# Optimization experiments

Measured on AMD Instinct MI355X. Metric: run time of the kernel, lower is better.

## Reference

```python
import jax, jax.numpy as jnp
import numpy as np

D_MODEL = 2048
NUM_HEADS = 16
D_Q = 1536
D_KV = 512
BS, SL = 2, 2048


def _lin(x, w, b):
    # torch nn.Linear: y = x @ w.T + b, w: [out, in]
    return jnp.einsum('...i,oi->...o', x, w) + b


def _freqs(seq_len, dim, theta=10000.0):
    # Faithful to source incl. precedence quirk: tn = 1 / ((theta ** arange) / dim).
    # float32 overflow -> inf -> tn = 0 for large exponents (identity rotation).
    exps = jnp.arange(0, dim, 2, dtype=jnp.float32)
    tn = 1.0 / ((theta ** exps) / dim)
    m = jnp.arange(seq_len, dtype=jnp.float32)
    ang = jnp.outer(m, tn)  # [sl, dim/2]
    return jnp.cos(ang), jnp.sin(ang)


def _rope(x, cos, sin):
    # x: [bs, sl, dim]; complex pairs are (x[..., 2i], x[..., 2i+1])
    xe = x[..., 0::2]
    xo = x[..., 1::2]
    re = xe * cos - xo * sin
    im = xe * sin + xo * cos
    return jnp.stack([re, im], axis=-1).reshape(x.shape)


def _init_linear(key, out_f, in_f):
    k1, k2 = jax.random.split(key)
    bound = 1.0 / np.sqrt(in_f)
    w = jax.random.uniform(k1, (out_f, in_f), jnp.float32, -bound, bound)
    b = jax.random.uniform(k2, (out_f,), jnp.float32, -bound, bound)
    return w, b


def setup_inputs() -> dict:
    key = jax.random.key(0)
    ks = jax.random.split(key, 9)
    x = jax.random.normal(ks[0], (BS, SL, D_MODEL), jnp.float32)
    w_down_q, b_down_q = _init_linear(ks[1], D_Q, D_MODEL)
    w_up_q, b_up_q = _init_linear(ks[2], D_MODEL, D_Q)
    w_down_kv, b_down_kv = _init_linear(ks[3], D_KV, D_MODEL)
    w_up_k, b_up_k = _init_linear(ks[4], D_MODEL, D_KV)
    w_up_v, b_up_v = _init_linear(ks[5], D_MODEL, D_KV)
    wq_r, bq_r = _init_linear(ks[6], D_MODEL, D_Q)
    wk_r, bk_r = _init_linear(ks[7], D_MODEL, D_KV)
    wo, bo = _init_linear(ks[8], D_MODEL, D_MODEL)
    return dict(x=x,
                w_down_q=w_down_q, b_down_q=b_down_q,
                w_up_q=w_up_q, b_up_q=b_up_q,
                w_down_kv=w_down_kv, b_down_kv=b_down_kv,
                w_up_k=w_up_k, b_up_k=b_up_k,
                w_up_v=w_up_v, b_up_v=b_up_v,
                wq_r=wq_r, bq_r=bq_r,
                wk_r=wk_r, bk_r=bk_r,
                wo=wo, bo=bo)


def reference(x, w_down_q, b_down_q, w_up_q, b_up_q, w_down_kv, b_down_kv,
              w_up_k, b_up_k, w_up_v, b_up_v, wq_r, bq_r, wk_r, bk_r, wo, bo):
    bs, sl, dim = x.shape
    nh, hd = NUM_HEADS, dim // NUM_HEADS
    cos, sin = _freqs(sl, dim)

    # Query path: down-proj -> up-proj content + decoupled RoPE branch
    ct_q = _lin(x, w_down_q, b_down_q)                       # [bs, sl, d_q]
    q_ct = _lin(ct_q, w_up_q, b_up_q)                        # [bs, sl, d_model]
    rope_q = _rope(_lin(ct_q, wq_r, bq_r), cos, sin)         # [bs, sl, d_model]
    q = (q_ct + rope_q).reshape(bs, sl, nh, hd)

    # KV path: shared latent -> separate K/V up-proj + RoPE branch on K
    ct_kv = _lin(x, w_down_kv, b_down_kv)                    # [bs, sl, d_kv]
    k_ct = _lin(ct_kv, w_up_k, b_up_k)
    rope_k = _rope(_lin(ct_kv, wk_r, bk_r), cos, sin)
    k = (k_ct + rope_k).reshape(bs, sl, nh, hd)
    v = _lin(ct_kv, w_up_v, b_up_v).reshape(bs, sl, nh, hd)

    # Attention: explicit matmul + softmax + matmul (no causal mask in source)
    scores = jnp.einsum('bqhd,bkhd->bhqk', q, k) / np.sqrt(hd)
    probs = jax.nn.softmax(scores, axis=-1)
    a = jnp.einsum('bhqk,bkhd->bqhd', probs, v).reshape(bs, sl, nh * hd)
    return _lin(a, wo, bo)
```

## Files before the change

### kernel.cpp

```cpp
#include <hip/hip_runtime.h>

typedef float f32x4 __attribute__((ext_vector_type(4)));
typedef unsigned short us8 __attribute__((ext_vector_type(8)));

#define DEVINL __device__ __forceinline__

DEVINL unsigned short f2bf(float f) {
  unsigned u = __builtin_bit_cast(unsigned, f);
  u += 0x7fffu + ((u >> 16) & 1u);
  return (unsigned short)(u >> 16);
}
DEVINL float bf2f(unsigned short b) { return __builtin_bit_cast(float, ((unsigned)b) << 16); }
DEVINL us8 ld8(const unsigned short* p) { return *reinterpret_cast<const us8*>(p); }
DEVINL void mfma_bf16(f32x4& acc, us8 a, us8 b) {
  asm("v_mfma_f32_16x16x32_bf16 %0, %1, %2, %0" : "+v"(acc) : "v"(a), "v"(b));
}
DEVINL unsigned cvtpk_bf16(float lo, float hi) {
  unsigned r;
  asm("v_cvt_pk_bf16_f32 %0, %1, %2" : "=v"(r) : "v"(lo), "v"(hi));
  return r;
}
DEVINL void gld16(const void* g, void* l) {
  __builtin_amdgcn_global_load_lds((const __attribute__((address_space(1))) void*)g,
                                   (__attribute__((address_space(3))) void*)l, 16, 0, 0);
}

__global__ void k_cvt(const float* __restrict__ in, unsigned short* __restrict__ out, int n4) {
  int i = blockIdx.x * 256 + threadIdx.x;
  if (i >= n4) return;
  float4 v = reinterpret_cast<const float4*>(in)[i];
  unsigned lo = (unsigned)f2bf(v.x) | ((unsigned)f2bf(v.y) << 16);
  unsigned hi = (unsigned)f2bf(v.z) | ((unsigned)f2bf(v.w) << 16);
  reinterpret_cast<uint2*>(out)[i] = make_uint2(lo, hi);
}

__global__ void k_freqs(float* __restrict__ cosT, float* __restrict__ sinT) {
  int idx = blockIdx.x * 256 + threadIdx.x;
  if (idx >= 2048 * 1024) return;
  int s = idx >> 10, i = idx & 1023;
  float e = (float)(2 * i);
  float pw = powf(10000.0f, e);
  float tn = 1.0f / (pw / 2048.0f);
  float ang = (float)s * tn;
  cosT[idx] = cosf(ang);
  sinT[idx] = sinf(ang);
}

template <bool OUTF32>
__global__ __launch_bounds__(256) void k_gemm_bt(const unsigned short* __restrict__ A,
                                                 const unsigned short* __restrict__ B,
                                                 const float* __restrict__ bias,
                                                 void* __restrict__ Cout, int M, int N, int K,
                                                 int lda) {
  __shared__ unsigned short As[128 * 32];
  __shared__ unsigned short Bs[128 * 32];
  const int nwg = gridDim.x;
  const int q8 = nwg >> 3;
  const int orig = blockIdx.x;
  const int wgid = (orig & 7) * q8 + (orig >> 3);
  const int nbn = N >> 7;
  const int bn = wgid % nbn, bm = wgid / nbn;
  const int tid = threadIdx.x, lane = tid & 63, w = tid >> 6;
  const int g = lane >> 4, l16 = lane & 15;
  const int wm = w >> 1, wn = w & 1;
  f32x4 acc[4][4] = {};
  const unsigned short* Arow = A + (size_t)bm * 128 * lda;
  const unsigned short* Brow = B + (size_t)bn * 128 * K;
  for (int kt = 0; kt < K; kt += 32) {
    __syncthreads();
#pragma unroll
    for (int j = 0; j < 2; ++j) {
      int c = (j * 4 + w) * 64 + lane;
      int row = c >> 2, c4 = c & 3;
      gld16(&Arow[(size_t)row * lda + kt + c4 * 8], &As[(j * 4 + w) * 64 * 8]);
      gld16(&Brow[(size_t)row * K + kt + c4 * 8], &Bs[(j * 4 + w) * 64 * 8]);
    }
    __syncthreads();
    us8 af[4], bfg[4];
#pragma unroll
    for (int mm = 0; mm < 4; ++mm) af[mm] = ld8(&As[(wm * 64 + mm * 16 + l16) * 32 + g * 8]);
#pragma unroll
    for (int nn = 0; nn < 4; ++nn) bfg[nn] = ld8(&Bs[(wn * 64 + nn * 16 + l16) * 32 + g * 8]);
#pragma unroll
    for (int mm = 0; mm < 4; ++mm)
#pragma unroll
      for (int nn = 0; nn < 4; ++nn) mfma_bf16(acc[mm][nn], af[mm], bfg[nn]);
  }
#pragma unroll
  for (int nn = 0; nn < 4; ++nn) {
    int col = bn * 128 + wn * 64 + nn * 16 + l16;
    float bv = bias[col];
#pragma unroll
    for (int mm = 0; mm < 4; ++mm) {
      int row0 = bm * 128 + wm * 64 + mm * 16 + g * 4;
#pragma unroll
      for (int r = 0; r < 4; ++r) {
        float vv = acc[mm][nn][r] + bv;
        if (OUTF32)
          reinterpret_cast<float*>(Cout)[(size_t)(row0 + r) * N + col] = vv;
        else
          reinterpret_cast<unsigned short*>(Cout)[(size_t)(row0 + r) * N + col] = f2bf(vv);
      }
    }
  }
}

__global__ void k_rope_combine(const unsigned short* __restrict__ src, int ldin,
                               const float* __restrict__ cosT, const float* __restrict__ sinT,
                               unsigned short* __restrict__ outp) {
  int pidx = blockIdx.x * 256 + threadIdx.x;
  if (pidx >= 4096 * 1024) return;
  int row = pidx >> 10, i = pidx & 1023;
  int s = row & 2047;
  float c = cosT[s * 1024 + i], sn = sinT[s * 1024 + i];
  const unsigned short* rp = src + (size_t)row * ldin;
  float xe = bf2f(rp[2048 + 2 * i]), xo = bf2f(rp[2048 + 2 * i + 1]);
  float re = xe * c - xo * sn;
  float im = xe * sn + xo * c;
  float q0 = bf2f(rp[2 * i]) + re;
  float q1 = bf2f(rp[2 * i + 1]) + im;
  unsigned pack = (unsigned)f2bf(q0) | ((unsigned)f2bf(q1) << 16);
  *reinterpret_cast<unsigned*>(&outp[(size_t)row * 2048 + 2 * i]) = pack;
}

__global__ __launch_bounds__(256) void k_transpose_v(const unsigned short* __restrict__ v, int ld,
                                                     unsigned short* __restrict__ vt) {
  __shared__ unsigned short t[32][33];
  int tx = threadIdx.x & 31, ty = threadIdx.x >> 5;
  int r0 = blockIdx.y * 32, c0 = blockIdx.x * 32;
#pragma unroll
  for (int jj = 0; jj < 4; ++jj)
    t[ty * 4 + jj][tx] = v[(size_t)(r0 + ty * 4 + jj) * ld + c0 + tx];
  __syncthreads();
  int b = r0 >> 11;
#pragma unroll
  for (int jj = 0; jj < 4; ++jj) {
    int colc = c0 + ty * 4 + jj;
    size_t orow = (size_t)(b * 16 + (colc >> 7)) * 128 + (colc & 127);
    vt[orow * 2048 + (r0 & 2047) + tx] = t[tx][ty * 4 + jj];
  }
}

__global__ __launch_bounds__(256, 2) void k_attn(const unsigned short* __restrict__ Q,
                                                 const unsigned short* __restrict__ Kg,
                                                 const unsigned short* __restrict__ VT,
                                                 unsigned short* __restrict__ Aout) {
  __shared__ unsigned short Ks[64 * 128];
  __shared__ unsigned short VTs[128 * 64];
  __shared__ unsigned short Ps[4][2][16 * 64];
  const int tid = threadIdx.x, lane = tid & 63, w = tid >> 6;
  const int g = lane >> 4, l16 = lane & 15;
  const int qt = blockIdx.x, h = blockIdx.y, b = blockIdx.z;
  const float SC2 = 0.08838834764831845f * 1.4426950408889634f;
  us8 qf[2][4];
#pragma unroll
  for (int qg = 0; qg < 2; ++qg) {
    const size_t qrow = (size_t)b * 2048 + qt * 128 + w * 32 + qg * 16 + l16;
#pragma unroll
    for (int kc = 0; kc < 4; ++kc)
      qf[qg][kc] = ld8(&Q[qrow * 2048 + h * 128 + kc * 32 + g * 8]);
  }
  f32x4 O[2][8] = {};
  float mq[2] = {-1e30f, -1e30f}, lq[2] = {0.f, 0.f};
  const unsigned short* Kbase = Kg + (size_t)b * 2048 * 2048 + h * 128;
  const unsigned short* VTb = VT + (size_t)(b * 16 + h) * 128 * 2048;
  for (int kt = 0; kt < 2048; kt += 64) {
    __syncthreads();
#pragma unroll
    for (int j = 0; j < 4; ++j) {
      int ch = (j * 4 + w) * 64 + lane;
      int key = ch >> 4, cp = ch & 15;
      gld16(&Kbase[(size_t)(kt + key) * 2048 + (size_t)((cp ^ (key & 7)) * 8)],
            &Ks[(j * 4 + w) * 64 * 8]);
      int d = ch >> 3, c2 = ch & 7;
      gld16(&VTb[(size_t)d * 2048 + kt + (size_t)((c2 ^ (d & 7)) * 8)],
            &VTs[(j * 4 + w) * 64 * 8]);
    }
    __syncthreads();
    f32x4 st[2][4] = {};
    __builtin_amdgcn_s_setprio(1);
#pragma unroll
    for (int t = 0; t < 4; ++t) {
      int key = t * 16 + l16;
      int swz = (key & 7) << 3;
#pragma unroll
      for (int kc = 0; kc < 4; ++kc) {
        us8 kf = ld8(&Ks[key * 128 + ((kc * 32 + g * 8) ^ swz)]);
        mfma_bf16(st[0][t], kf, qf[0][kc]);
        mfma_bf16(st[1][t], kf, qf[1][kc]);
      }
    }
    __builtin_amdgcn_s_setprio(0);
    const int qswz = (l16 & 7) << 3;
#pragma unroll
    for (int qg = 0; qg < 2; ++qg) {
      float sv[16];
      float smax = -1e30f;
#pragma unroll
      for (int t = 0; t < 4; ++t)
#pragma unroll
        for (int r = 0; r < 4; ++r) {
          sv[t * 4 + r] = st[qg][t][r] * SC2;
          smax = fmaxf(smax, sv[t * 4 + r]);
        }
      smax = fmaxf(smax, __shfl_xor(smax, 16));
      smax = fmaxf(smax, __shfl_xor(smax, 32));
      float mn = fmaxf(mq[qg], smax);
      float fac = exp2f(mq[qg] - mn);
      float ps = 0.f;
#pragma unroll
      for (int i = 0; i < 16; ++i) {
        sv[i] = exp2f(sv[i] - mn);
        ps += sv[i];
      }
      ps += __shfl_xor(ps, 16);
      ps += __shfl_xor(ps, 32);
      lq[qg] = lq[qg] * fac + ps;
      mq[qg] = mn;
#pragma unroll
      for (int r = 0; r < 4; ++r) {
        float fr = __shfl(fac, g * 4 + r);
#pragma unroll
        for (int n0 = 0; n0 < 8; ++n0) O[qg][n0][r] *= fr;
      }
      unsigned* P32 = reinterpret_cast<unsigned*>(&Ps[w][qg][0]);
#pragma unroll
      for (int t = 0; t < 4; ++t)
#pragma unroll
        for (int pp = 0; pp < 2; ++pp) {
          int key = t * 16 + g * 4 + pp * 2;
          unsigned pk = cvtpk_bf16(sv[t * 4 + pp * 2], sv[t * 4 + pp * 2 + 1]);
          int elem = l16 * 64 + (key ^ qswz);
          P32[elem >> 1] = pk;
        }
    }
    us8 pf[2][2];
#pragma unroll
    for (int qg = 0; qg < 2; ++qg)
#pragma unroll
      for (int kc = 0; kc < 2; ++kc)
        pf[qg][kc] = ld8(&Ps[w][qg][l16 * 64 + ((kc * 32 + g * 8) ^ qswz)]);
    __builtin_amdgcn_s_setprio(1);
#pragma unroll
    for (int n0 = 0; n0 < 8; ++n0) {
      int d = n0 * 16 + l16;
      int dsw = (d & 7) << 3;
#pragma unroll
      for (int kc = 0; kc < 2; ++kc) {
        us8 vf = ld8(&VTs[d * 64 + ((kc * 32 + g * 8) ^ dsw)]);
        mfma_bf16(O[0][n0], pf[0][kc], vf);
        mfma_bf16(O[1][n0], pf[1][kc], vf);
      }
    }
    __builtin_amdgcn_s_setprio(0);
  }
#pragma unroll
  for (int qg = 0; qg < 2; ++qg) {
    float inv = 1.0f / lq[qg];
#pragma unroll
    for (int r = 0; r < 4; ++r) {
      float ir = __shfl(inv, g * 4 + r);
      size_t row = (size_t)b * 2048 + qt * 128 + w * 32 + qg * 16 + g * 4 + r;
#pragma unroll
      for (int n0 = 0; n0 < 8; ++n0)
        Aout[row * 2048 + h * 128 + n0 * 16 + l16] = f2bf(O[qg][n0][r] * ir);
    }
  }
}

extern "C" void kernel_launch(void* const* d_in, const int* in_sizes, int n_in, void* d_out,
                              int out_size, void* d_ws, size_t ws_size, hipStream_t stream) {
  (void)in_sizes; (void)n_in; (void)out_size; (void)ws_size;
  constexpr int Mr = 4096;
  using US = unsigned short;
  const float* x        = (const float*)d_in[0];
  const float* w_down_q = (const float*)d_in[1];
  const float* b_down_q = (const float*)d_in[2];
  const float* w_up_q   = (const float*)d_in[3];
  const float* b_up_q   = (const float*)d_in[4];
  const float* w_down_kv= (const float*)d_in[5];
  const float* b_down_kv= (const float*)d_in[6];
  const float* w_up_k   = (const float*)d_in[7];
  const float* b_up_k   = (const float*)d_in[8];
  const float* w_up_v   = (const float*)d_in[9];
  const float* b_up_v   = (const float*)d_in[10];
  const float* wq_r     = (const float*)d_in[11];
  const float* bq_r     = (const float*)d_in[12];
  const float* wk_r     = (const float*)d_in[13];
  const float* bk_r     = (const float*)d_in[14];
  const float* wo       = (const float*)d_in[15];
  const float* bo       = (const float*)d_in[16];

  char* p = (char*)d_ws;
  auto alloc = [&](size_t bytes) { char* r = p; p += (bytes + 255) & ~(size_t)255; return r; };
  float* cosT = (float*)alloc((size_t)2048 * 1024 * 4);
  float* sinT = (float*)alloc((size_t)2048 * 1024 * 4);
  US* xb        = (US*)alloc((size_t)Mr * 2048 * 2);
  US* wcat_down = (US*)alloc((size_t)2048 * 2048 * 2);
  US* wcat_qup  = (US*)alloc((size_t)4096 * 1536 * 2);
  US* wcat_kvup = (US*)alloc((size_t)6144 * 512 * 2);
  US* wob       = (US*)alloc((size_t)2048 * 2048 * 2);
  US* ct        = (US*)alloc((size_t)Mr * 2048 * 2);
  US* big       = (US*)alloc((size_t)Mr * 6144 * 2);
  US* vtb       = (US*)alloc((size_t)Mr * 2048 * 2);
  float* bcat_down = (float*)alloc(2048 * 4);
  float* bcat_qup  = (float*)alloc(4096 * 4);
  float* bcat_kvup = (float*)alloc(6144 * 4);
  US* qb   = xb;
  US* kb   = wcat_down;
  US* t12  = big;
  US* kv3  = big;
  US* aout = ct;

  auto cvt = [&](const float* s, US* dptr, size_t n) {
    int n4 = (int)(n / 4);
    k_cvt<<<dim3((n4 + 255) / 256), dim3(256), 0, stream>>>(s, dptr, n4);
  };
  cvt(x, xb, (size_t)Mr * 2048);
  cvt(w_down_q, wcat_down, (size_t)1536 * 2048);
  cvt(w_down_kv, wcat_down + (size_t)1536 * 2048, (size_t)512 * 2048);
  cvt(w_up_q, wcat_qup, (size_t)2048 * 1536);
  cvt(wq_r, wcat_qup + (size_t)2048 * 1536, (size_t)2048 * 1536);
  cvt(w_up_k, wcat_kvup, (size_t)2048 * 512);
  cvt(wk_r, wcat_kvup + (size_t)2048 * 512, (size_t)2048 * 512);
  cvt(w_up_v, wcat_kvup + (size_t)4096 * 512, (size_t)2048 * 512);
  cvt(wo, wob, (size_t)2048 * 2048);
  hipMemcpyAsync(bcat_down, b_down_q, 1536 * 4, hipMemcpyDeviceToDevice, stream);
  hipMemcpyAsync(bcat_down + 1536, b_down_kv, 512 * 4, hipMemcpyDeviceToDevice, stream);
  hipMemcpyAsync(bcat_qup, b_up_q, 2048 * 4, hipMemcpyDeviceToDevice, stream);
  hipMemcpyAsync(bcat_qup + 2048, bq_r, 2048 * 4, hipMemcpyDeviceToDevice, stream);
  hipMemcpyAsync(bcat_kvup, b_up_k, 2048 * 4, hipMemcpyDeviceToDevice, stream);
  hipMemcpyAsync(bcat_kvup + 2048, bk_r, 2048 * 4, hipMemcpyDeviceToDevice, stream);
  hipMemcpyAsync(bcat_kvup + 4096, b_up_v, 2048 * 4, hipMemcpyDeviceToDevice, stream);
  k_freqs<<<dim3((2048 * 1024 + 255) / 256), dim3(256), 0, stream>>>(cosT, sinT);

  auto gemm_bf = [&](const US* A, const US* B, const float* bias, US* C, int M, int N, int K,
                     int lda) {
    k_gemm_bt<false><<<dim3((N / 128) * (M / 128)), dim3(256), 0, stream>>>(A, B, bias, (void*)C,
                                                                            M, N, K, lda);
  };
  gemm_bf(xb, wcat_down, bcat_down, ct, Mr, 2048, 2048, 2048);
  gemm_bf(ct, wcat_qup, bcat_qup, t12, Mr, 4096, 1536, 2048);
  k_rope_combine<<<dim3((4096 * 1024 + 255) / 256), dim3(256), 0, stream>>>(t12, 4096, cosT, sinT,
                                                                            qb);
  gemm_bf(ct + 1536, wcat_kvup, bcat_kvup, kv3, Mr, 6144, 512, 2048);
  k_rope_combine<<<dim3((4096 * 1024 + 255) / 256), dim3(256), 0, stream>>>(kv3, 6144, cosT, sinT,
                                                                            kb);
  k_transpose_v<<<dim3(64, 128), dim3(256), 0, stream>>>(kv3 + 4096, 6144, vtb);
  k_attn<<<dim3(16, 16, 2), dim3(256), 0, stream>>>(qb, kb, vtb, aout);
  k_gemm_bt<true><<<dim3((2048 / 128) * (Mr / 128)), dim3(256), 0, stream>>>(aout, wob, bo, d_out,
                                                                             Mr, 2048, 2048, 2048);
}
```

Before: 412.0 us.

## Double-buffer attention K/V, lazy softmax rescale, fold scale into Q, narrower GEMM tiles

The attention kernel now double-buffers its K and V^T shared-memory tiles, so the next tile's global-to-LDS load overlaps compute on the current one. Online-softmax rescaling of O and l is skipped unless the running max grows by more than 8 (in log2 units). The softmax scale is folded into Q during rope_combine. The GEMM gains a BN template parameter, and the N=2048 GEMMs use 64-wide tiles for more workgroups. Doubled LDS in attention may reduce occupancy, and the lazy rescale lets unnormalised exponentials grow up to 2^8, which risks precision loss in the bf16 P values.

```diff
diff --git a/kernel.cpp b/kernel.cpp
--- a/kernel.cpp
+++ b/kernel.cpp
@@ -46,49 +46,56 @@
   sinT[idx] = sinf(ang);
 }
 
-template <bool OUTF32>
+template <int BN, bool OUTF32>
 __global__ __launch_bounds__(256) void k_gemm_bt(const unsigned short* __restrict__ A,
                                                  const unsigned short* __restrict__ B,
                                                  const float* __restrict__ bias,
                                                  void* __restrict__ Cout, int M, int N, int K,
                                                  int lda) {
+  constexpr int NN = BN / 32;
   __shared__ unsigned short As[128 * 32];
-  __shared__ unsigned short Bs[128 * 32];
+  __shared__ unsigned short Bs[BN * 32];
   const int nwg = gridDim.x;
   const int q8 = nwg >> 3;
   const int orig = blockIdx.x;
   const int wgid = (orig & 7) * q8 + (orig >> 3);
-  const int nbn = N >> 7;
+  const int nbn = N / BN;
   const int bn = wgid % nbn, bm = wgid / nbn;
   const int tid = threadIdx.x, lane = tid & 63, w = tid >> 6;
   const int g = lane >> 4, l16 = lane & 15;
   const int wm = w >> 1, wn = w & 1;
-  f32x4 acc[4][4] = {};
+  f32x4 acc[4][NN] = {};
   const unsigned short* Arow = A + (size_t)bm * 128 * lda;
-  const unsigned short* Brow = B + (size_t)bn * 128 * K;
+  const unsigned short* Brow = B + (size_t)bn * BN * K;
   for (int kt = 0; kt < K; kt += 32) {
     __syncthreads();
 #pragma unroll
     for (int j = 0; j < 2; ++j) {
       int c = (j * 4 + w) * 64 + lane;
       int row = c >> 2, c4 = c & 3;
-      gld16(&Arow[(size_t)row * lda + kt + c4 * 8], &As[(j * 4 + w) * 64 * 8]);
-      gld16(&Brow[(size_t)row * K + kt + c4 * 8], &Bs[(j * 4 + w) * 64 * 8]);
+      gld16(&Arow[(size_t)row * lda + kt + c4 * 8], &As[(j * 4 + w) * 512]);
+    }
+#pragma unroll
+    for (int jb = 0; jb < BN / 64; ++jb) {
+      int c = (jb * 4 + w) * 64 + lane;
+      int row = c >> 2, c4 = c & 3;
+      gld16(&Brow[(size_t)row * K + kt + c4 * 8], &Bs[(jb * 4 + w) * 512]);
     }
     __syncthreads();
-    us8 af[4], bfg[4];
+    us8 af[4], bfg[NN];
 #pragma unroll
     for (int mm = 0; mm < 4; ++mm) af[mm] = ld8(&As[(wm * 64 + mm * 16 + l16) * 32 + g * 8]);
 #pragma unroll
-    for (int nn = 0; nn < 4; ++nn) bfg[nn] = ld8(&Bs[(wn * 64 + nn * 16 + l16) * 32 + g * 8]);
+    for (int nn = 0; nn < NN; ++nn)
+      bfg[nn] = ld8(&Bs[(wn * (BN / 2) + nn * 16 + l16) * 32 + g * 8]);
 #pragma unroll
     for (int mm = 0; mm < 4; ++mm)
 #pragma unroll
-      for (int nn = 0; nn < 4; ++nn) mfma_bf16(acc[mm][nn], af[mm], bfg[nn]);
-  }
-#pragma unroll
-  for (int nn = 0; nn < 4; ++nn) {
-    int col = bn * 128 + wn * 64 + nn * 16 + l16;
+      for (int nn = 0; nn < NN; ++nn) mfma_bf16(acc[mm][nn], af[mm], bfg[nn]);
+  }
+#pragma unroll
+  for (int nn = 0; nn < NN; ++nn) {
+    int col = bn * BN + wn * (BN / 2) + nn * 16 + l16;
     float bv = bias[col];
 #pragma unroll
     for (int mm = 0; mm < 4; ++mm) {
@@ -105,7 +112,7 @@
   }
 }
 
-__global__ void k_rope_combine(const unsigned short* __restrict__ src, int ldin,
+__global__ void k_rope_combine(const unsigned short* __restrict__ src, int ldin, float oscale,
                                const float* __restrict__ cosT, const float* __restrict__ sinT,
                                unsigned short* __restrict__ outp) {
   int pidx = blockIdx.x * 256 + threadIdx.x;
@@ -117,8 +124,8 @@
   float xe = bf2f(rp[2048 + 2 * i]), xo = bf2f(rp[2048 + 2 * i + 1]);
   float re = xe * c - xo * sn;
   float im = xe * sn + xo * c;
-  float q0 = bf2f(rp[2 * i]) + re;
-  float q1 = bf2f(rp[2 * i + 1]) + im;
+  float q0 = (bf2f(rp[2 * i]) + re) * oscale;
+  float q1 = (bf2f(rp[2 * i + 1]) + im) * oscale;
   unsigned pack = (unsigned)f2bf(q0) | ((unsigned)f2bf(q1) << 16);
   *reinterpret_cast<unsigned*>(&outp[(size_t)row * 2048 + 2 * i]) = pack;
 }
@@ -145,13 +152,12 @@
                                                  const unsigned short* __restrict__ Kg,
                                                  const unsigned short* __restrict__ VT,
                                                  unsigned short* __restrict__ Aout) {
-  __shared__ unsigned short Ks[64 * 128];
-  __shared__ unsigned short VTs[128 * 64];
+  __shared__ unsigned short Ks[2][64 * 128];
+  __shared__ unsigned short VTs[2][128 * 64];
   __shared__ unsigned short Ps[4][2][16 * 64];
   const int tid = threadIdx.x, lane = tid & 63, w = tid >> 6;
   const int g = lane >> 4, l16 = lane & 15;
   const int qt = blockIdx.x, h = blockIdx.y, b = blockIdx.z;
-  const float SC2 = 0.08838834764831845f * 1.4426950408889634f;
   us8 qf[2][4];
 #pragma unroll
   for (int qg = 0; qg < 2; ++qg) {
@@ -164,30 +170,38 @@
   float mq[2] = {-1e30f, -1e30f}, lq[2] = {0.f, 0.f};
   const unsigned short* Kbase = Kg + (size_t)b * 2048 * 2048 + h * 128;
   const unsigned short* VTb = VT + (size_t)(b * 16 + h) * 128 * 2048;
-  for (int kt = 0; kt < 2048; kt += 64) {
-    __syncthreads();
+
+  auto STAGE = [&](int bufi, int ktrow) {
 #pragma unroll
     for (int j = 0; j < 4; ++j) {
       int ch = (j * 4 + w) * 64 + lane;
       int key = ch >> 4, cp = ch & 15;
-      gld16(&Kbase[(size_t)(kt + key) * 2048 + (size_t)((cp ^ (key & 7)) * 8)],
-            &Ks[(j * 4 + w) * 64 * 8]);
+      gld16(&Kbase[(size_t)(ktrow + key) * 2048 + (size_t)((cp ^ (key & 7)) * 8)],
+            &Ks[bufi][(j * 4 + w) * 512]);
       int d = ch >> 3, c2 = ch & 7;
-      gld16(&VTb[(size_t)d * 2048 + kt + (size_t)((c2 ^ (d & 7)) * 8)],
-            &VTs[(j * 4 + w) * 64 * 8]);
-    }
+      gld16(&VTb[(size_t)d * 2048 + ktrow + (size_t)((c2 ^ (d & 7)) * 8)],
+            &VTs[bufi][(j * 4 + w) * 512]);
+    }
+  };
+
+  STAGE(0, 0);
+  for (int t = 0; t < 32; ++t) {
+    const int cur = t & 1;
     __syncthreads();
+    if (t < 31) STAGE(cur ^ 1, (t + 1) * 64);
+    const unsigned short* KsC = &Ks[cur][0];
+    const unsigned short* VTsC = &VTs[cur][0];
     f32x4 st[2][4] = {};
     __builtin_amdgcn_s_setprio(1);
 #pragma unroll
-    for (int t = 0; t < 4; ++t) {
-      int key = t * 16 + l16;
+    for (int tt = 0; tt < 4; ++tt) {
+      int key = tt * 16 + l16;
       int swz = (key & 7) << 3;
 #pragma unroll
       for (int kc = 0; kc < 4; ++kc) {
-        us8 kf = ld8(&Ks[key * 128 + ((kc * 32 + g * 8) ^ swz)]);
-        mfma_bf16(st[0][t], kf, qf[0][kc]);
-        mfma_bf16(st[1][t], kf, qf[1][kc]);
+        us8 kf = ld8(&KsC[key * 128 + ((kc * 32 + g * 8) ^ swz)]);
+        mfma_bf16(st[0][tt], kf, qf[0][kc]);
+        mfma_bf16(st[1][tt], kf, qf[1][kc]);
       }
     }
     __builtin_amdgcn_s_setprio(0);
@@ -197,16 +211,28 @@
       float sv[16];
       float smax = -1e30f;
 #pragma unroll
-      for (int t = 0; t < 4; ++t)
+      for (int tt = 0; tt < 4; ++tt)
 #pragma unroll
         for (int r = 0; r < 4; ++r) {
-          sv[t * 4 + r] = st[qg][t][r] * SC2;
-          smax = fmaxf(smax, sv[t * 4 + r]);
+          sv[tt * 4 + r] = st[qg][tt][r];
+          smax = fmaxf(smax, sv[tt * 4 + r]);
         }
       smax = fmaxf(smax, __shfl_xor(smax, 16));
       smax = fmaxf(smax, __shfl_xor(smax, 32));
-      float mn = fmaxf(mq[qg], smax);
-      float fac = exp2f(mq[qg] - mn);
+      float mo = mq[qg];
+      if (!__all(smax <= mo + 8.0f)) {
+        float mn = fmaxf(mo, smax);
+        float fac = exp2f(mo - mn);
+        lq[qg] *= fac;
+        mq[qg] = mn;
+#pragma unroll
+        for (int r = 0; r < 4; ++r) {
+          float fr = __shfl(fac, g * 4 + r);
+#pragma unroll
+          for (int n0 = 0; n0 < 8; ++n0) O[qg][n0][r] *= fr;
+        }
+      }
+      float mn = mq[qg];
       float ps = 0.f;
 #pragma unroll
       for (int i = 0; i < 16; ++i) {
@@ -215,21 +241,14 @@
       }
       ps += __shfl_xor(ps, 16);
       ps += __shfl_xor(ps, 32);
-      lq[qg] = lq[qg] * fac + ps;
-      mq[qg] = mn;
-#pragma unroll
-      for (int r = 0; r < 4; ++r) {
-        float fr = __shfl(fac, g * 4 + r);
-#pragma unroll
-        for (int n0 = 0; n0 < 8; ++n0) O[qg][n0][r] *= fr;
-      }
+      lq[qg] += ps;
       unsigned* P32 = reinterpret_cast<unsigned*>(&Ps[w][qg][0]);
 #pragma unroll
-      for (int t = 0; t < 4; ++t)
+      for (int tt = 0; tt < 4; ++tt)
 #pragma unroll
         for (int pp = 0; pp < 2; ++pp) {
-          int key = t * 16 + g * 4 + pp * 2;
-          unsigned pk = cvtpk_bf16(sv[t * 4 + pp * 2], sv[t * 4 + pp * 2 + 1]);
+          int key = tt * 16 + g * 4 + pp * 2;
+          unsigned pk = cvtpk_bf16(sv[tt * 4 + pp * 2], sv[tt * 4 + pp * 2 + 1]);
           int elem = l16 * 64 + (key ^ qswz);
           P32[elem >> 1] = pk;
         }
@@ -247,7 +266,7 @@
       int dsw = (d & 7) << 3;
 #pragma unroll
       for (int kc = 0; kc < 2; ++kc) {
-        us8 vf = ld8(&VTs[d * 64 + ((kc * 32 + g * 8) ^ dsw)]);
+        us8 vf = ld8(&VTsC[d * 64 + ((kc * 32 + g * 8) ^ dsw)]);
         mfma_bf16(O[0][n0], pf[0][kc], vf);
         mfma_bf16(O[1][n0], pf[1][kc], vf);
       }
@@ -334,20 +353,20 @@
   hipMemcpyAsync(bcat_kvup + 4096, b_up_v, 2048 * 4, hipMemcpyDeviceToDevice, stream);
   k_freqs<<<dim3((2048 * 1024 + 255) / 256), dim3(256), 0, stream>>>(cosT, sinT);
 
-  auto gemm_bf = [&](const US* A, const US* B, const float* bias, US* C, int M, int N, int K,
-                     int lda) {
-    k_gemm_bt<false><<<dim3((N / 128) * (M / 128)), dim3(256), 0, stream>>>(A, B, bias, (void*)C,
-                                                                            M, N, K, lda);
-  };
-  gemm_bf(xb, wcat_down, bcat_down, ct, Mr, 2048, 2048, 2048);
-  gemm_bf(ct, wcat_qup, bcat_qup, t12, Mr, 4096, 1536, 2048);
-  k_rope_combine<<<dim3((4096 * 1024 + 255) / 256), dim3(256), 0, stream>>>(t12, 4096, cosT, sinT,
-                                                                            qb);
-  gemm_bf(ct + 1536, wcat_kvup, bcat_kvup, kv3, Mr, 6144, 512, 2048);
-  k_rope_combine<<<dim3((4096 * 1024 + 255) / 256), dim3(256), 0, stream>>>(kv3, 6144, cosT, sinT,
-                                                                            kb);
+  const float SCQ = 0.08838834764831845f * 1.4426950408889634f;
+
+  k_gemm_bt<64, false><<<dim3((2048 / 64) * (Mr / 128)), dim3(256), 0, stream>>>(
+      xb, wcat_down, bcat_down, (void*)ct, Mr, 2048, 2048, 2048);
+  k_gemm_bt<128, false><<<dim3((4096 / 128) * (Mr / 128)), dim3(256), 0, stream>>>(
+      ct, wcat_qup, bcat_qup, (void*)t12, Mr, 4096, 1536, 2048);
+  k_rope_combine<<<dim3((4096 * 1024 + 255) / 256), dim3(256), 0, stream>>>(t12, 4096, SCQ, cosT,
+                                                                            sinT, qb);
+  k_gemm_bt<128, false><<<dim3((6144 / 128) * (Mr / 128)), dim3(256), 0, stream>>>(
+      ct + 1536, wcat_kvup, bcat_kvup, (void*)kv3, Mr, 6144, 512, 2048);
+  k_rope_combine<<<dim3((4096 * 1024 + 255) / 256), dim3(256), 0, stream>>>(kv3, 6144, 1.0f, cosT,
+                                                                            sinT, kb);
   k_transpose_v<<<dim3(64, 128), dim3(256), 0, stream>>>(kv3 + 4096, 6144, vtb);
   k_attn<<<dim3(16, 16, 2), dim3(256), 0, stream>>>(qb, kb, vtb, aout);
-  k_gemm_bt<true><<<dim3((2048 / 128) * (Mr / 128)), dim3(256), 0, stream>>>(aout, wob, bo, d_out,
-                                                                             Mr, 2048, 2048, 2048);
-}
+  k_gemm_bt<64, true><<<dim3((2048 / 64) * (Mr / 128)), dim3(256), 0, stream>>>(
+      aout, wob, bo, d_out, Mr, 2048, 2048, 2048);
+}
```

Result: no change. 416.4 us (+1.1%).
